# Kernel optimization log

Hardware: AMD Instinct MI355X
Metric: run time of the kernel (lower is better)

Reference implementation:

```python
import jax, jax.numpy as jnp
import numpy as np

N, C, K, P, Q, PS = 32, 128, 128, 64, 64, 3

def setup_inputs() -> dict:
    key = jax.random.key(0)
    k1, k2, k3 = jax.random.split(key, 3)
    x = jax.random.normal(k1, (N, C, P, Q), dtype=jnp.float32)
    W = jax.random.normal(k2, (K, C * PS * PS), dtype=jnp.float32) * (1.0 / np.sqrt(C * PS * PS))
    perturbs = jax.random.normal(k3, (N, K, P, Q), dtype=jnp.float32)
    return {"x": x, "W": W, "perturbs": perturbs}

def reference(x, W, perturbs):
    # patchify (pad=1, unfold 3x3, stride 1) + matmul with W^T is exactly a
    # 3x3 SAME convolution: flatten order of patchify is (C, kh, kw), matching
    # conv.weight.reshape(k, -1). Express it as a direct conv (no im2col blowup).
    k = W.shape[0]
    c = x.shape[1]
    w = W.reshape(k, c, PS, PS)  # OIHW
    out = jax.lax.conv_general_dilated(
        x, w,
        window_strides=(1, 1),
        padding=((1, 1), (1, 1)),
        dimension_numbers=("NCHW", "OIHW", "NCHW"),
    )
    return out + perturbs
```

## Files before the change

kernel.cpp:

```cpp
#include <hip/hip_runtime.h>
#include <hip/hip_bf16.h>

#define NN 32
#define CCH 128
#define KK 128
#define PP 64
#define QQ 64

typedef __bf16 bf16x8 __attribute__((ext_vector_type(8)));
typedef float f32x16 __attribute__((ext_vector_type(16)));
typedef float f32x4 __attribute__((ext_vector_type(4)));

#define XT_ELEMS (32ull * 64 * 64 * 128)

__global__ __launch_bounds__(256) void prep_x(const float* __restrict__ x,
                                              __bf16* __restrict__ xT) {
    __shared__ float tile[128 * 64];
    const int t = threadIdx.x;
    const int p = blockIdx.x;
    const int n = blockIdx.y;

#pragma unroll
    for (int pass = 0; pass < 8; ++pass) {
        int idx = pass * 256 + t;
        int qf = idx & 15;
        int c  = idx >> 4;
        f32x4 v = *(const f32x4*)(x + (((size_t)n * CCH + c) * PP + p) * QQ + qf * 4);
        int key = ((c >> 3) & 15) * 4;
        *(f32x4*)(tile + c * 64 + ((qf * 4) ^ key)) = v;
    }
    __syncthreads();

#pragma unroll
    for (int pass = 0; pass < 4; ++pass) {
        int cc   = pass * 2 + (t >> 7);
        int rem  = t & 127;
        int q    = rem >> 1;
        int half = rem & 1;
        int c0   = cc * 16 + half * 8;
        int key  = ((c0 >> 3) & 15) * 4;
        bf16x8 o;
#pragma unroll
        for (int j = 0; j < 8; ++j) o[j] = (__bf16)tile[(c0 + j) * 64 + (q ^ key)];
        *(bf16x8*)(xT + ((((size_t)n * 8 + cc) * PP + p) * QQ + q) * 16 + half * 8) = o;
    }
}

__global__ __launch_bounds__(256) void prep_w(const float* __restrict__ W,
                                              __bf16* __restrict__ Wf) {
    const int id = blockIdx.x * 256 + threadIdx.x;
    const int lane = id & 63;
    const int r1   = id >> 6;
    const int kb   = r1 & 3;
    const int r2   = r1 >> 2;
    const int t    = r2 % 9;
    const int cc   = r2 / 9;

    const int k  = kb * 32 + (lane & 31);
    const int c0 = cc * 16 + (lane >> 5) * 8;

    bf16x8 o;
#pragma unroll
    for (int j = 0; j < 8; ++j)
        o[j] = (__bf16)W[(size_t)k * (CCH * 9) + (size_t)(c0 + j) * 9 + t];
    ((bf16x8*)Wf)[id] = o;
}

#define XPITCH 2112
__global__ __launch_bounds__(256, 2) void conv_main(const __bf16* __restrict__ xT,
                                                    const __bf16* __restrict__ Wf,
                                                    const float* __restrict__ per,
                                                    float* __restrict__ out) {
    __shared__ __align__(16) char wlds[36864];
    __shared__ __align__(16) char xlds[6 * XPITCH];

    const int tid  = threadIdx.x;
    const int lane = tid & 63;
    const int w    = tid >> 6;
    const int kbs  = w & 1;
    const int pb2  = w >> 1;
    const int n    = blockIdx.y;
    const int p0   = blockIdx.x * 4;
    const int m    = lane & 31;
    const int half = lane >> 5;

    if (tid < 24) {
        int row = tid >> 2, part = tid & 3;
        int off = row * XPITCH + (part >> 1) * 2080 + (part & 1) * 16;
        *(f32x4*)(xlds + off) = f32x4{0.f, 0.f, 0.f, 0.f};
    }

    f32x16 acc[2][2][2];
#pragma unroll
    for (int a = 0; a < 2; ++a)
#pragma unroll
        for (int b = 0; b < 2; ++b)
#pragma unroll
            for (int c = 0; c < 2; ++c)
#pragma unroll
                for (int e = 0; e < 16; ++e) acc[a][b][c][e] = 0.f;

    const char* xb = (const char*)xT + ((size_t)n * 8) * PP * QQ * 32;

    for (int cc = 0; cc < 8; ++cc) {
        __syncthreads();
        {
            const char* g = (const char*)Wf + (size_t)cc * 36864;
#pragma unroll
            for (int it = 0; it < 9; ++it) {
                int off = (it * 256 + tid) * 16;
                __builtin_amdgcn_global_load_lds(
                    (const __attribute__((address_space(1))) unsigned int*)(g + off),
                    (__attribute__((address_space(3))) unsigned int*)(wlds + off),
                    16, 0, 0);
            }
        }
        {
            const char* gx = xb + (size_t)cc * (PP * QQ * 32);
#pragma unroll
            for (int it = 0; it < 3; ++it) {
                int gi  = it * 256 + tid;
                int row = gi >> 7;
                int wi  = (gi & 127) * 16;
                int r   = p0 - 1 + row;
                int rc  = r < 0 ? 0 : (r > 63 ? 63 : r);
                __builtin_amdgcn_global_load_lds(
                    (const __attribute__((address_space(1))) unsigned int*)(gx + (size_t)rc * 2048 + wi),
                    (__attribute__((address_space(3))) unsigned int*)(xlds + row * XPITCH + 32 + wi),
                    16, 0, 0);
            }
        }
        __syncthreads();

        bf16x8 a_cur[3][2], a_prev[3][2];
#pragma unroll
        for (int ri = 0; ri < 4; ++ri) {
            const int rr = pb2 * 2 + ri;
            const int r  = p0 + pb2 * 2 + ri - 1;
            const bool rok = ((unsigned)r < (unsigned)PP);

            bf16x8 b[3][2];
            if (rok) {
                const char* rbase = xlds + rr * XPITCH + half * 16;
#pragma unroll
                for (int dq = 0; dq < 3; ++dq)
#pragma unroll
                    for (int qb = 0; qb < 2; ++qb)
                        b[dq][qb] = *(const bf16x8*)(rbase + (qb * 32 + m + dq) * 32);
            }

            if (ri < 3) {
#pragma unroll
                for (int dq = 0; dq < 3; ++dq)
#pragma unroll
                    for (int kb = 0; kb < 2; ++kb)
                        a_cur[dq][kb] = ((const bf16x8*)wlds)[((ri * 3 + dq) * 4 +
                                                               kbs * 2 + kb) * 64 + lane];
            }

            if (rok) {
                if (ri >= 1) {
#pragma unroll
                    for (int dq = 0; dq < 3; ++dq)
#pragma unroll
                        for (int kb = 0; kb < 2; ++kb)
#pragma unroll
                            for (int qb = 0; qb < 2; ++qb)
                                acc[1][kb][qb] = __builtin_amdgcn_mfma_f32_32x32x16_bf16(
                                    a_prev[dq][kb], b[dq][qb], acc[1][kb][qb], 0, 0, 0);
                }
                if (ri < 3) {
#pragma unroll
                    for (int dq = 0; dq < 3; ++dq)
#pragma unroll
                        for (int kb = 0; kb < 2; ++kb)
#pragma unroll
                            for (int qb = 0; qb < 2; ++qb)
                                acc[0][kb][qb] = __builtin_amdgcn_mfma_f32_32x32x16_bf16(
                                    a_cur[dq][kb], b[dq][qb], acc[0][kb][qb], 0, 0, 0);
                }
            }

            if (ri < 3) {
#pragma unroll
                for (int dq = 0; dq < 3; ++dq)
#pragma unroll
                    for (int kb = 0; kb < 2; ++kb) a_prev[dq][kb] = a_cur[dq][kb];
            }
        }
    }

#pragma unroll
    for (int oi = 0; oi < 2; ++oi) {
        const int prow = p0 + pb2 * 2 + oi;
#pragma unroll
        for (int kbi = 0; kbi < 2; ++kbi) {
#pragma unroll
            for (int qb = 0; qb < 2; ++qb) {
                f32x16 v = acc[oi][kbi][qb];
#pragma unroll
                for (int r = 0; r < 16; ++r) {
                    int krow = (r & 3) + 8 * (r >> 2) + 4 * half;
                    int k    = (kbs * 2 + kbi) * 32 + krow;
                    int q    = qb * 32 + m;
                    size_t oidx = (((size_t)n * KK + k) * PP + prow) * QQ + q;
                    out[oidx] = v[r] + per[oidx];
                }
            }
        }
    }
}

extern "C" void kernel_launch(void* const* d_in, const int* in_sizes, int n_in,
                              void* d_out, int out_size, void* d_ws, size_t ws_size,
                              hipStream_t stream) {
    const float* x   = (const float*)d_in[0];
    const float* W   = (const float*)d_in[1];
    const float* per = (const float*)d_in[2];
    float* out = (float*)d_out;

    __bf16* xT = (__bf16*)d_ws;
    __bf16* Wf = (__bf16*)((char*)d_ws + XT_ELEMS * 2);

    prep_x<<<dim3(PP, NN), 256, 0, stream>>>(x, xT);
    prep_w<<<dim3(72), 256, 0, stream>>>(W, Wf);
    conv_main<<<dim3(PP / 4, NN), 256, 0, stream>>>(xT, Wf, per, out);
}
```

Baseline: 208.7 us.

## Double-buffer LDS staging and grow conv block to 8 rows with 512 threads

Weight and input tiles now go into two LDS buffers, so the next channel chunk is loaded while MFMA runs on the current one. Each block also covers 8 output rows with 8 waves instead of 4 rows with 4 waves, so each weight tile fetch is shared by more output rows. The grid halves to 256 blocks and LDS per block roughly doubles to about 116 KB, which likely limits residency to one block per CU. The only wait before a buffer is reused is the barrier at the end of each iteration, and there is no explicit wait on the asynchronous global-to-LDS loads before the data is consumed.

```diff
diff --git a/kernel.cpp b/kernel.cpp
--- a/kernel.cpp
+++ b/kernel.cpp
@@ -67,27 +67,32 @@
 }
 
 #define XPITCH 2112
-__global__ __launch_bounds__(256, 2) void conv_main(const __bf16* __restrict__ xT,
+#define WBYTES 36864
+#define XROWS  10
+#define XBYTES (XROWS * XPITCH)
+
+__global__ __launch_bounds__(512, 2) void conv_main(const __bf16* __restrict__ xT,
                                                     const __bf16* __restrict__ Wf,
                                                     const float* __restrict__ per,
                                                     float* __restrict__ out) {
-    __shared__ __align__(16) char wlds[36864];
-    __shared__ __align__(16) char xlds[6 * XPITCH];
+    __shared__ __align__(16) char wlds[2][WBYTES];
+    __shared__ __align__(16) char xlds[2][XBYTES];
 
     const int tid  = threadIdx.x;
     const int lane = tid & 63;
     const int w    = tid >> 6;
     const int kbs  = w & 1;
-    const int pb2  = w >> 1;
+    const int pb   = w >> 1;
     const int n    = blockIdx.y;
-    const int p0   = blockIdx.x * 4;
+    const int p0   = blockIdx.x * 8;
     const int m    = lane & 31;
     const int half = lane >> 5;
 
-    if (tid < 24) {
+    if (tid < 40) {
         int row = tid >> 2, part = tid & 3;
         int off = row * XPITCH + (part >> 1) * 2080 + (part & 1) * 16;
-        *(f32x4*)(xlds + off) = f32x4{0.f, 0.f, 0.f, 0.f};
+        *(f32x4*)(xlds[0] + off) = f32x4{0.f, 0.f, 0.f, 0.f};
+        *(f32x4*)(xlds[1] + off) = f32x4{0.f, 0.f, 0.f, 0.f};
     }
 
     f32x16 acc[2][2][2];
@@ -102,46 +107,55 @@
 
     const char* xb = (const char*)xT + ((size_t)n * 8) * PP * QQ * 32;
 
-    for (int cc = 0; cc < 8; ++cc) {
-        __syncthreads();
-        {
-            const char* g = (const char*)Wf + (size_t)cc * 36864;
-#pragma unroll
-            for (int it = 0; it < 9; ++it) {
-                int off = (it * 256 + tid) * 16;
+    auto stage = [&](int ccn, int buf) {
+        const char* g = (const char*)Wf + (size_t)ccn * WBYTES;
+#pragma unroll
+        for (int it = 0; it < 5; ++it) {
+            int idx = it * 512 + tid;
+            if (idx < WBYTES / 16) {
                 __builtin_amdgcn_global_load_lds(
-                    (const __attribute__((address_space(1))) unsigned int*)(g + off),
-                    (__attribute__((address_space(3))) unsigned int*)(wlds + off),
+                    (const __attribute__((address_space(1))) unsigned int*)(g + idx * 16),
+                    (__attribute__((address_space(3))) unsigned int*)(wlds[buf] + idx * 16),
                     16, 0, 0);
             }
         }
-        {
-            const char* gx = xb + (size_t)cc * (PP * QQ * 32);
-#pragma unroll
-            for (int it = 0; it < 3; ++it) {
-                int gi  = it * 256 + tid;
+        const char* gx = xb + (size_t)ccn * (PP * QQ * 32);
+#pragma unroll
+        for (int it = 0; it < 3; ++it) {
+            int gi = it * 512 + tid;
+            if (gi < XROWS * 128) {
                 int row = gi >> 7;
                 int wi  = (gi & 127) * 16;
                 int r   = p0 - 1 + row;
                 int rc  = r < 0 ? 0 : (r > 63 ? 63 : r);
                 __builtin_amdgcn_global_load_lds(
                     (const __attribute__((address_space(1))) unsigned int*)(gx + (size_t)rc * 2048 + wi),
-                    (__attribute__((address_space(3))) unsigned int*)(xlds + row * XPITCH + 32 + wi),
+                    (__attribute__((address_space(3))) unsigned int*)(xlds[buf] + row * XPITCH + 32 + wi),
                     16, 0, 0);
             }
         }
-        __syncthreads();
+    };
+
+    stage(0, 0);
+    __syncthreads();
+
+    int cur = 0;
+    for (int cc = 0; cc < 8; ++cc) {
+        if (cc < 7) stage(cc + 1, cur ^ 1);
+
+        const char* wbase = wlds[cur];
+        const char* xbase = xlds[cur];
 
         bf16x8 a_cur[3][2], a_prev[3][2];
 #pragma unroll
         for (int ri = 0; ri < 4; ++ri) {
-            const int rr = pb2 * 2 + ri;
-            const int r  = p0 + pb2 * 2 + ri - 1;
+            const int rr = pb * 2 + ri;
+            const int r  = p0 + pb * 2 + ri - 1;
             const bool rok = ((unsigned)r < (unsigned)PP);
 
             bf16x8 b[3][2];
             if (rok) {
-                const char* rbase = xlds + rr * XPITCH + half * 16;
+                const char* rbase = xbase + rr * XPITCH + half * 16;
 #pragma unroll
                 for (int dq = 0; dq < 3; ++dq)
 #pragma unroll
@@ -154,8 +168,8 @@
                 for (int dq = 0; dq < 3; ++dq)
 #pragma unroll
                     for (int kb = 0; kb < 2; ++kb)
-                        a_cur[dq][kb] = ((const bf16x8*)wlds)[((ri * 3 + dq) * 4 +
-                                                               kbs * 2 + kb) * 64 + lane];
+                        a_cur[dq][kb] = ((const bf16x8*)wbase)[((ri * 3 + dq) * 4 +
+                                                                kbs * 2 + kb) * 64 + lane];
             }
 
             if (rok) {
@@ -188,11 +202,14 @@
                     for (int kb = 0; kb < 2; ++kb) a_prev[dq][kb] = a_cur[dq][kb];
             }
         }
+
+        __syncthreads();
+        cur ^= 1;
     }
 
 #pragma unroll
     for (int oi = 0; oi < 2; ++oi) {
-        const int prow = p0 + pb2 * 2 + oi;
+        const int prow = p0 + pb * 2 + oi;
 #pragma unroll
         for (int kbi = 0; kbi < 2; ++kbi) {
 #pragma unroll
@@ -224,5 +241,5 @@
 
     prep_x<<<dim3(PP, NN), 256, 0, stream>>>(x, xT);
     prep_w<<<dim3(72), 256, 0, stream>>>(W, Wf);
-    conv_main<<<dim3(PP / 4, NN), 256, 0, stream>>>(xT, Wf, per, out);
-}
+    conv_main<<<dim3(PP / 8, NN), 512, 0, stream>>>(xT, Wf, per, out);
+}
```

New measurement: 214.4 us. 1.03x slower.
